# Kernel tuning notes

Hardware: AMD Instinct MI355X
Metric: run time of the kernel (lower is better)

The kernel has to match this reference:

```python
import jax, jax.numpy as jnp
import numpy as np

WH, WW = 7, 7
N = WH * WW
NH = 6
HEAD_DIM = 192 // NH
W_RES = 56
R_MAX = 4 * 56  # patch_size[0] * H
PI = 3.141592653589793


def _rel_coords():
    ch, cw = np.arange(WH), np.arange(WW)
    coords = np.stack(np.meshgrid(ch, cw, indexing='ij'))  # (2, WH, WW)
    flat = coords.reshape(2, -1)
    rel = flat[:, :, None] - flat[:, None, :]  # (2, N, N)
    radius = rel[0]   # in [-(WH-1), WH-1]
    azimuth = rel[1]  # in [-(WW-1), WW-1]
    return radius, azimuth


def setup_inputs() -> dict:
    key = jax.random.key(0)
    ks = jax.random.split(key, 10)
    B_ = 2048
    dim = 192
    return {
        'x': jax.random.normal(ks[0], (B_, N, dim), jnp.float32),
        'D': jax.random.uniform(ks[1], (B_, 1), jnp.float32),
        'qkv_w': jax.random.normal(ks[2], (3 * dim, dim), jnp.float32) * 0.02,
        'qkv_b': jax.random.normal(ks[3], (3 * dim,), jnp.float32) * 0.02,
        'proj_w': jax.random.normal(ks[4], (dim, dim), jnp.float32) * 0.02,
        'proj_b': jax.random.normal(ks[5], (dim,), jnp.float32) * 0.02,
        'a_p': jax.random.normal(ks[6], (2 * WW - 1, NH), jnp.float32) * 0.02,
        'b_p': jax.random.normal(ks[7], (2 * WW - 1, NH), jnp.float32) * 0.02,
        'a_r': jax.random.normal(ks[8], (2 * WH - 1, NH), jnp.float32) * 0.02,
        'b_r': jax.random.normal(ks[9], (2 * WH - 1, NH), jnp.float32) * 0.02,
    }


def reference(x, D, qkv_w, qkv_b, proj_w, proj_b, a_p, b_p, a_r, b_r):
    B_, n, C = x.shape
    radius_np, azimuth_np = _rel_coords()
    # torch a_r[radius] with negative ints wraps like python indexing; emulate via modulo
    rad_idx = jnp.asarray(radius_np % (2 * WH - 1))
    az_idx = jnp.asarray(azimuth_np % (2 * WW - 1))
    radius = jnp.asarray(radius_np, jnp.float32)   # (N, N)
    azimuth = jnp.asarray(azimuth_np, jnp.float32)  # (N, N)

    scale = HEAD_DIM ** -0.5
    qkv = (x @ qkv_w.T + qkv_b).reshape(B_, n, 3, NH, HEAD_DIM)
    qkv = jnp.transpose(qkv, (2, 0, 3, 1, 4))  # (3, B_, NH, N, hd)
    q, k, v = qkv[0] * scale, qkv[1], qkv[2]

    attn = jnp.einsum('bhnd,bhmd->bhnm', q, k)  # (B_, NH, N, N)

    # azimuthal bias: (N, N, NH) -> (NH, N, N)
    az = azimuth * (2.0 * PI / W_RES)
    A_phi = a_p[az_idx] * jnp.cos(az)[..., None] + b_p[az_idx] * jnp.sin(az)[..., None]
    A_phi = jnp.transpose(A_phi, (2, 0, 1))  # (NH, N, N)

    # radial bias: D (B_,1) scales radius -> (B_, N, N); combine -> (B_, NH, N, N)
    rad = D[:, 0][:, None, None] * radius[None]  # (B_, N, N)
    ang = rad * (2.0 * PI / R_MAX)
    A_r = (a_r[rad_idx][None] * jnp.cos(ang)[..., None]
           + b_r[rad_idx][None] * jnp.sin(ang)[..., None])  # (B_, N, N, NH)
    A_r = jnp.transpose(A_r, (0, 3, 1, 2))  # (B_, NH, N, N)

    attn = jax.nn.softmax(attn + A_phi[None] + A_r, axis=-1)
    out = jnp.einsum('bhnm,bhmd->bhnd', attn, v)
    out = jnp.transpose(out, (0, 2, 1, 3)).reshape(B_, n, C)
    return out @ proj_w.T + proj_b
```

## Files before the change

kernel.cpp:

```cpp
#include <hip/hip_runtime.h>

#define NTOK 49
#define NH 6
#define HD 32
#define DIM 192
#define QKV_DIM 576
#define PI_F 3.14159265358979323846f

typedef __bf16 bf16_t;
typedef __bf16 bf16x4 __attribute__((ext_vector_type(4)));
typedef __bf16 bf16x8 __attribute__((ext_vector_type(8)));
typedef float f32x4 __attribute__((ext_vector_type(4)));

__global__ __launch_bounds__(256) void cvt_weights(const float* __restrict__ qkv_w,
                                                   const float* __restrict__ proj_w,
                                                   bf16_t* __restrict__ wq,
                                                   bf16_t* __restrict__ wp) {
    int idx = blockIdx.x * 256 + threadIdx.x;
    if (idx < QKV_DIM * DIM) {
        wq[idx] = (bf16_t)qkv_w[idx];
    } else {
        int j = idx - QKV_DIM * DIM;
        if (j < DIM * DIM) wp[j] = (bf16_t)proj_w[j];
    }
}

__global__ __launch_bounds__(384) void fused_win_attn(
        const float* __restrict__ x,
        const float* __restrict__ Dp,
        const bf16_t* __restrict__ wq,
        const float* __restrict__ qkv_b,
        const bf16_t* __restrict__ wp,
        const float* __restrict__ proj_b,
        const float* __restrict__ a_p,
        const float* __restrict__ b_p,
        const float* __restrict__ a_r,
        const float* __restrict__ b_r,
        float* __restrict__ out) {
    __shared__ __align__(16) bf16_t sh_xo[64 * 200];
    __shared__ __align__(16) bf16_t q_sh[NH][64 * 40];
    __shared__ __align__(16) bf16_t k_sh[NH][64 * 40];
    __shared__ __align__(16) bf16_t vt_sh[NH][32 * 72];
    __shared__ __align__(16) bf16_t P_sh[NH][16 * 72];
    __shared__ float bias_sh[NH][169];

    const int tid  = threadIdx.x;
    const int w    = tid >> 6;
    const int lane = tid & 63;
    const int l16  = lane & 15;
    const int quad = lane >> 4;
    const int win  = blockIdx.x;

    bf16_t* q_lds  = q_sh[w];
    bf16_t* k_lds  = k_sh[w];
    bf16_t* vt     = vt_sh[w];
    bf16_t* P      = P_sh[w];
    float*  bias13 = bias_sh[w];

    const float* xg = x + (size_t)win * (NTOK * DIM);
    for (int u = tid; u < 2352; u += 384) {
        int e = u * 4;
        int r = e / 192, c = e % 192;
        float4 xv = *(const float4*)(xg + e);
        bf16x4 pk = { (bf16_t)xv.x, (bf16_t)xv.y, (bf16_t)xv.z, (bf16_t)xv.w };
        *(bf16x4*)(&sh_xo[r * 200 + c]) = pk;
    }
    {
        bf16x8 z = {};
        for (int u = tid; u < 360; u += 384) {
            int e = u * 8;
            int r = 49 + e / 192, c = e % 192;
            *(bf16x8*)(&sh_xo[r * 200 + c]) = z;
        }
    }
    __syncthreads();

    bf16x8 af[4][6];
#pragma unroll
    for (int mt = 0; mt < 4; ++mt)
#pragma unroll
        for (int ks = 0; ks < 6; ++ks)
            af[mt][ks] = *(const bf16x8*)(&sh_xo[(mt * 16 + l16) * 200 + ks * 32 + quad * 8]);
    __syncthreads();

    const float Dv = Dp[win];
    for (int u = lane; u < 169; u += 64) {
        int dr = u / 13 - 6, da = u % 13 - 6;
        int ri = (dr < 0) ? dr + 13 : dr;
        int ai = (da < 0) ? da + 13 : da;
        float ang_a = (float)da * (2.0f * PI_F / 56.0f);
        float ang_r = Dv * (float)dr * (2.0f * PI_F / 448.0f);
        bias13[u] = a_p[ai * NH + w] * __cosf(ang_a) + b_p[ai * NH + w] * __sinf(ang_a)
                  + a_r[ri * NH + w] * __cosf(ang_r) + b_r[ri * NH + w] * __sinf(ang_r);
    }

    const float scale = 0.17677669529663687f;
    for (int part = 0; part < 3; ++part) {
        const int base_c = part * DIM + w * 32;
        const bf16_t* wg = wq + (size_t)base_c * DIM;
        f32x4 acc[4][2] = {};
#pragma unroll
        for (int ks = 0; ks < 6; ++ks) {
            bf16x8 b0 = *(const bf16x8*)(wg + (size_t)l16 * DIM + ks * 32 + quad * 8);
            bf16x8 b1 = *(const bf16x8*)(wg + (size_t)(16 + l16) * DIM + ks * 32 + quad * 8);
#pragma unroll
            for (int mt = 0; mt < 4; ++mt) {
                acc[mt][0] = __builtin_amdgcn_mfma_f32_16x16x32_bf16(af[mt][ks], b0, acc[mt][0], 0, 0, 0);
                acc[mt][1] = __builtin_amdgcn_mfma_f32_16x16x32_bf16(af[mt][ks], b1, acc[mt][1], 0, 0, 0);
            }
        }
        float bb0 = qkv_b[base_c + l16];
        float bb1 = qkv_b[base_c + 16 + l16];
        if (part == 0) {
#pragma unroll
            for (int mt = 0; mt < 4; ++mt)
#pragma unroll
                for (int r = 0; r < 4; ++r) {
                    int tok = mt * 16 + quad * 4 + r;
                    q_lds[tok * 40 + l16]      = (bf16_t)((acc[mt][0][r] + bb0) * scale);
                    q_lds[tok * 40 + 16 + l16] = (bf16_t)((acc[mt][1][r] + bb1) * scale);
                }
        } else if (part == 1) {
#pragma unroll
            for (int mt = 0; mt < 4; ++mt)
#pragma unroll
                for (int r = 0; r < 4; ++r) {
                    int tok = mt * 16 + quad * 4 + r;
                    k_lds[tok * 40 + l16]      = (bf16_t)(acc[mt][0][r] + bb0);
                    k_lds[tok * 40 + 16 + l16] = (bf16_t)(acc[mt][1][r] + bb1);
                }
        } else {
#pragma unroll
            for (int mt = 0; mt < 4; ++mt)
#pragma unroll
                for (int r = 0; r < 4; ++r) {
                    int tok = mt * 16 + quad * 4 + r;
                    vt[(l16) * 72 + tok]      = (bf16_t)(acc[mt][0][r] + bb0);
                    vt[(16 + l16) * 72 + tok] = (bf16_t)(acc[mt][1][r] + bb1);
                }
        }
    }

    bf16x8 kf[4];
#pragma unroll
    for (int nt = 0; nt < 4; ++nt)
        kf[nt] = *(const bf16x8*)(&k_lds[(nt * 16 + l16) * 40 + quad * 8]);
    bf16x8 vf[2][2];
#pragma unroll
    for (int ntd = 0; ntd < 2; ++ntd)
#pragma unroll
        for (int kt = 0; kt < 2; ++kt)
            vf[ntd][kt] = *(const bf16x8*)(&vt[(ntd * 16 + l16) * 72 + kt * 32 + quad * 8]);

    int jh[4], jw[4];
#pragma unroll
    for (int nt = 0; nt < 4; ++nt) {
        int j = nt * 16 + l16;
        jh[nt] = j / 7;
        jw[nt] = j - 7 * jh[nt];
    }

    for (int mt = 0; mt < 4; ++mt) {
        bf16x8 qf = *(const bf16x8*)(&q_lds[(mt * 16 + l16) * 40 + quad * 8]);

        f32x4 s[4] = {};
#pragma unroll
        for (int nt = 0; nt < 4; ++nt)
            s[nt] = __builtin_amdgcn_mfma_f32_16x16x32_bf16(qf, kf[nt], s[nt], 0, 0, 0);

        float ev[4][4];
        float rs[4];
#pragma unroll
        for (int r = 0; r < 4; ++r) {
            int i = mt * 16 + quad * 4 + r;
            int ih = i / 7, iw = i - 7 * ih;
            float val[4];
            float mx = -1e30f;
#pragma unroll
            for (int nt = 0; nt < 4; ++nt) {
                int j = nt * 16 + l16;
                int idx = (ih - jh[nt] + 6) * 13 + (iw - jw[nt] + 6);
                idx = min(max(idx, 0), 168);
                float vv = s[nt][r] + bias13[idx];
                if (j >= 49) vv = -1e30f;
                val[nt] = vv;
                mx = fmaxf(mx, vv);
            }
#pragma unroll
            for (int m = 1; m <= 8; m <<= 1) mx = fmaxf(mx, __shfl_xor(mx, m));
            float sum = 0.f;
#pragma unroll
            for (int nt = 0; nt < 4; ++nt) {
                float e = __expf(val[nt] - mx);
                ev[r][nt] = e;
                sum += e;
            }
#pragma unroll
            for (int m = 1; m <= 8; m <<= 1) sum += __shfl_xor(sum, m);
            rs[r] = 1.0f / sum;
        }

#pragma unroll
        for (int r = 0; r < 4; ++r)
#pragma unroll
            for (int nt = 0; nt < 4; ++nt)
                P[(quad * 4 + r) * 72 + nt * 16 + l16] = (bf16_t)ev[r][nt];

        bf16x8 pa[2];
#pragma unroll
        for (int kt = 0; kt < 2; ++kt)
            pa[kt] = *(const bf16x8*)(&P[l16 * 72 + kt * 32 + quad * 8]);

        f32x4 o[2] = {};
#pragma unroll
        for (int ntd = 0; ntd < 2; ++ntd)
#pragma unroll
            for (int kt = 0; kt < 2; ++kt)
                o[ntd] = __builtin_amdgcn_mfma_f32_16x16x32_bf16(pa[kt], vf[ntd][kt], o[ntd], 0, 0, 0);

#pragma unroll
        for (int r = 0; r < 4; ++r) {
            int tok = mt * 16 + quad * 4 + r;
            bf16_t* op = &sh_xo[tok * 200 + w * 32];
            op[l16]      = (bf16_t)(o[0][r] * rs[r]);
            op[16 + l16] = (bf16_t)(o[1][r] * rs[r]);
        }
    }

    __syncthreads();

    bf16x8 wf[2][6];
#pragma unroll
    for (int nt = 0; nt < 2; ++nt)
#pragma unroll
        for (int ks = 0; ks < 6; ++ks)
            wf[nt][ks] = *(const bf16x8*)(wp + (size_t)(w * 32 + nt * 16 + l16) * DIM + ks * 32 + quad * 8);

    f32x4 pacc[4][2] = {};
#pragma unroll
    for (int mt = 0; mt < 4; ++mt)
#pragma unroll
        for (int ks = 0; ks < 6; ++ks) {
            bf16x8 oa = *(const bf16x8*)(&sh_xo[(mt * 16 + l16) * 200 + ks * 32 + quad * 8]);
#pragma unroll
            for (int nt = 0; nt < 2; ++nt)
                pacc[mt][nt] = __builtin_amdgcn_mfma_f32_16x16x32_bf16(oa, wf[nt][ks], pacc[mt][nt], 0, 0, 0);
        }

    float pb0 = proj_b[w * 32 + l16];
    float pb1 = proj_b[w * 32 + 16 + l16];
#pragma unroll
    for (int mt = 0; mt < 4; ++mt)
#pragma unroll
        for (int r = 0; r < 4; ++r) {
            int i = mt * 16 + quad * 4 + r;
            if (i < 49) {
                float* op = out + ((size_t)win * NTOK + i) * DIM + w * 32;
                op[l16]      = pacc[mt][0][r] + pb0;
                op[16 + l16] = pacc[mt][1][r] + pb1;
            }
        }
}

extern "C" void kernel_launch(void* const* d_in, const int* in_sizes, int n_in,
                              void* d_out, int out_size, void* d_ws, size_t ws_size,
                              hipStream_t stream) {
    const float* x      = (const float*)d_in[0];
    const float* D      = (const float*)d_in[1];
    const float* qkv_w  = (const float*)d_in[2];
    const float* qkv_b  = (const float*)d_in[3];
    const float* proj_w = (const float*)d_in[4];
    const float* proj_b = (const float*)d_in[5];
    const float* a_p    = (const float*)d_in[6];
    const float* b_p    = (const float*)d_in[7];
    const float* a_r    = (const float*)d_in[8];
    const float* b_r    = (const float*)d_in[9];
    float* out = (float*)d_out;

    const int B_ = in_sizes[0] / (NTOK * DIM);

    char* wsp = (char*)d_ws;
    bf16_t* wq = (bf16_t*)wsp; wsp += (size_t)QKV_DIM * DIM * 2;
    bf16_t* wp = (bf16_t*)wsp;

    cvt_weights<<<dim3((QKV_DIM * DIM + DIM * DIM + 255) / 256), dim3(256), 0, stream>>>(
        qkv_w, proj_w, wq, wp);

    fused_win_attn<<<dim3(B_), dim3(384), 0, stream>>>(
        x, D, wq, qkv_b, wp, proj_b, a_p, b_p, a_r, b_r, out);
}
```

Before: 293.2 us.

## Keep Q/K/P in registers via transposed MFMA and lane shuffles, shrink LDS

Computes Q and K transposed (weights as the A operand) and rebuilds their MFMA fragments with cross-lane shuffles instead of staging them through LDS. Softmax now runs down columns, and P is rebuilt through shuffles too, so the Q, K and P shared buffers go away. The x tile is no longer held in registers and is instead re-read from LDS with clamped rows. Launch bounds now request 3 blocks per CU. Together these cut LDS footprint and register pressure to raise occupancy, at the cost of more shuffle instructions and repeated LDS reads of x.

```diff
diff --git a/kernel.cpp b/kernel.cpp
--- a/kernel.cpp
+++ b/kernel.cpp
@@ -25,7 +25,27 @@
     }
 }
 
-__global__ __launch_bounds__(384) void fused_win_attn(
+__device__ __forceinline__ int2 pack4(float a, float b, float c, float d) {
+    bf16x4 t = { (bf16_t)a, (bf16_t)b, (bf16_t)c, (bf16_t)d };
+    union { bf16x4 v; int2 i; } u;
+    u.v = t;
+    return u.i;
+}
+
+__device__ __forceinline__ bf16x8 asm_frag(int2 p0, int2 p1, int src_lo, bool sel_hi) {
+    int a0x = __shfl(p0.x, src_lo),      a0y = __shfl(p0.y, src_lo);
+    int a1x = __shfl(p0.x, src_lo + 16), a1y = __shfl(p0.y, src_lo + 16);
+    int b0x = __shfl(p1.x, src_lo),      b0y = __shfl(p1.y, src_lo);
+    int b1x = __shfl(p1.x, src_lo + 16), b1y = __shfl(p1.y, src_lo + 16);
+    union { int x[4]; bf16x8 v; } u;
+    u.x[0] = sel_hi ? b0x : a0x;
+    u.x[1] = sel_hi ? b0y : a0y;
+    u.x[2] = sel_hi ? b1x : a1x;
+    u.x[3] = sel_hi ? b1y : a1y;
+    return u.v;
+}
+
+__global__ __launch_bounds__(384, 3) void fused_win_attn(
         const float* __restrict__ x,
         const float* __restrict__ Dp,
         const bf16_t* __restrict__ wq,
@@ -37,11 +57,8 @@
         const float* __restrict__ a_r,
         const float* __restrict__ b_r,
         float* __restrict__ out) {
-    __shared__ __align__(16) bf16_t sh_xo[64 * 200];
-    __shared__ __align__(16) bf16_t q_sh[NH][64 * 40];
-    __shared__ __align__(16) bf16_t k_sh[NH][64 * 40];
+    __shared__ __align__(16) bf16_t sh_xo[49 * 200];
     __shared__ __align__(16) bf16_t vt_sh[NH][32 * 72];
-    __shared__ __align__(16) bf16_t P_sh[NH][16 * 72];
     __shared__ float bias_sh[NH][169];
 
     const int tid  = threadIdx.x;
@@ -51,10 +68,7 @@
     const int quad = lane >> 4;
     const int win  = blockIdx.x;
 
-    bf16_t* q_lds  = q_sh[w];
-    bf16_t* k_lds  = k_sh[w];
     bf16_t* vt     = vt_sh[w];
-    bf16_t* P      = P_sh[w];
     float*  bias13 = bias_sh[w];
 
     const float* xg = x + (size_t)win * (NTOK * DIM);
@@ -65,23 +79,6 @@
         bf16x4 pk = { (bf16_t)xv.x, (bf16_t)xv.y, (bf16_t)xv.z, (bf16_t)xv.w };
         *(bf16x4*)(&sh_xo[r * 200 + c]) = pk;
     }
-    {
-        bf16x8 z = {};
-        for (int u = tid; u < 360; u += 384) {
-            int e = u * 8;
-            int r = 49 + e / 192, c = e % 192;
-            *(bf16x8*)(&sh_xo[r * 200 + c]) = z;
-        }
-    }
-    __syncthreads();
-
-    bf16x8 af[4][6];
-#pragma unroll
-    for (int mt = 0; mt < 4; ++mt)
-#pragma unroll
-        for (int ks = 0; ks < 6; ++ks)
-            af[mt][ks] = *(const bf16x8*)(&sh_xo[(mt * 16 + l16) * 200 + ks * 32 + quad * 8]);
-    __syncthreads();
 
     const float Dv = Dp[win];
     for (int u = lane; u < 169; u += 64) {
@@ -93,58 +90,85 @@
         bias13[u] = a_p[ai * NH + w] * __cosf(ang_a) + b_p[ai * NH + w] * __sinf(ang_a)
                   + a_r[ri * NH + w] * __cosf(ang_r) + b_r[ri * NH + w] * __sinf(ang_r);
     }
+    __syncthreads();
+
+    int xoff[4];
+#pragma unroll
+    for (int mt = 0; mt < 4; ++mt) {
+        int row = mt * 16 + l16;
+        xoff[mt] = min(row, 48) * 200 + quad * 8;
+    }
 
     const float scale = 0.17677669529663687f;
-    for (int part = 0; part < 3; ++part) {
-        const int base_c = part * DIM + w * 32;
-        const bf16_t* wg = wq + (size_t)base_c * DIM;
-        f32x4 acc[4][2] = {};
+    int2 qp[4][2], kp[4][2];
+    {
+        const bf16_t* wgq = wq + (size_t)(w * 32) * DIM;
+        const bf16_t* wgk = wq + (size_t)(DIM + w * 32) * DIM;
+        f32x4 qa[4][2] = {}, ka[4][2] = {};
 #pragma unroll
         for (int ks = 0; ks < 6; ++ks) {
-            bf16x8 b0 = *(const bf16x8*)(wg + (size_t)l16 * DIM + ks * 32 + quad * 8);
-            bf16x8 b1 = *(const bf16x8*)(wg + (size_t)(16 + l16) * DIM + ks * 32 + quad * 8);
+            bf16x8 wq0 = *(const bf16x8*)(wgq + (size_t)l16 * DIM + ks * 32 + quad * 8);
+            bf16x8 wq1 = *(const bf16x8*)(wgq + (size_t)(16 + l16) * DIM + ks * 32 + quad * 8);
+            bf16x8 wk0 = *(const bf16x8*)(wgk + (size_t)l16 * DIM + ks * 32 + quad * 8);
+            bf16x8 wk1 = *(const bf16x8*)(wgk + (size_t)(16 + l16) * DIM + ks * 32 + quad * 8);
 #pragma unroll
             for (int mt = 0; mt < 4; ++mt) {
-                acc[mt][0] = __builtin_amdgcn_mfma_f32_16x16x32_bf16(af[mt][ks], b0, acc[mt][0], 0, 0, 0);
-                acc[mt][1] = __builtin_amdgcn_mfma_f32_16x16x32_bf16(af[mt][ks], b1, acc[mt][1], 0, 0, 0);
-            }
-        }
-        float bb0 = qkv_b[base_c + l16];
-        float bb1 = qkv_b[base_c + 16 + l16];
-        if (part == 0) {
-#pragma unroll
-            for (int mt = 0; mt < 4; ++mt)
-#pragma unroll
-                for (int r = 0; r < 4; ++r) {
-                    int tok = mt * 16 + quad * 4 + r;
-                    q_lds[tok * 40 + l16]      = (bf16_t)((acc[mt][0][r] + bb0) * scale);
-                    q_lds[tok * 40 + 16 + l16] = (bf16_t)((acc[mt][1][r] + bb1) * scale);
-                }
-        } else if (part == 1) {
-#pragma unroll
-            for (int mt = 0; mt < 4; ++mt)
-#pragma unroll
-                for (int r = 0; r < 4; ++r) {
-                    int tok = mt * 16 + quad * 4 + r;
-                    k_lds[tok * 40 + l16]      = (bf16_t)(acc[mt][0][r] + bb0);
-                    k_lds[tok * 40 + 16 + l16] = (bf16_t)(acc[mt][1][r] + bb1);
-                }
-        } else {
-#pragma unroll
-            for (int mt = 0; mt < 4; ++mt)
-#pragma unroll
-                for (int r = 0; r < 4; ++r) {
-                    int tok = mt * 16 + quad * 4 + r;
-                    vt[(l16) * 72 + tok]      = (bf16_t)(acc[mt][0][r] + bb0);
-                    vt[(16 + l16) * 72 + tok] = (bf16_t)(acc[mt][1][r] + bb1);
-                }
-        }
-    }
-
-    bf16x8 kf[4];
-#pragma unroll
-    for (int nt = 0; nt < 4; ++nt)
-        kf[nt] = *(const bf16x8*)(&k_lds[(nt * 16 + l16) * 40 + quad * 8]);
+                bf16x8 xf = *(const bf16x8*)(&sh_xo[xoff[mt] + ks * 32]);
+                qa[mt][0] = __builtin_amdgcn_mfma_f32_16x16x32_bf16(wq0, xf, qa[mt][0], 0, 0, 0);
+                qa[mt][1] = __builtin_amdgcn_mfma_f32_16x16x32_bf16(wq1, xf, qa[mt][1], 0, 0, 0);
+                ka[mt][0] = __builtin_amdgcn_mfma_f32_16x16x32_bf16(wk0, xf, ka[mt][0], 0, 0, 0);
+                ka[mt][1] = __builtin_amdgcn_mfma_f32_16x16x32_bf16(wk1, xf, ka[mt][1], 0, 0, 0);
+            }
+        }
+        float4 bq0 = *(const float4*)(qkv_b + w * 32 + quad * 4);
+        float4 bq1 = *(const float4*)(qkv_b + w * 32 + 16 + quad * 4);
+        float4 bk0 = *(const float4*)(qkv_b + DIM + w * 32 + quad * 4);
+        float4 bk1 = *(const float4*)(qkv_b + DIM + w * 32 + 16 + quad * 4);
+#pragma unroll
+        for (int mt = 0; mt < 4; ++mt) {
+            qp[mt][0] = pack4((qa[mt][0][0] + bq0.x) * scale, (qa[mt][0][1] + bq0.y) * scale,
+                              (qa[mt][0][2] + bq0.z) * scale, (qa[mt][0][3] + bq0.w) * scale);
+            qp[mt][1] = pack4((qa[mt][1][0] + bq1.x) * scale, (qa[mt][1][1] + bq1.y) * scale,
+                              (qa[mt][1][2] + bq1.z) * scale, (qa[mt][1][3] + bq1.w) * scale);
+            kp[mt][0] = pack4(ka[mt][0][0] + bk0.x, ka[mt][0][1] + bk0.y,
+                              ka[mt][0][2] + bk0.z, ka[mt][0][3] + bk0.w);
+            kp[mt][1] = pack4(ka[mt][1][0] + bk1.x, ka[mt][1][1] + bk1.y,
+                              ka[mt][1][2] + bk1.z, ka[mt][1][3] + bk1.w);
+        }
+    }
+    {
+        const bf16_t* wgv = wq + (size_t)(2 * DIM + w * 32) * DIM;
+        f32x4 va[4][2] = {};
+#pragma unroll
+        for (int ks = 0; ks < 6; ++ks) {
+            bf16x8 wv0 = *(const bf16x8*)(wgv + (size_t)l16 * DIM + ks * 32 + quad * 8);
+            bf16x8 wv1 = *(const bf16x8*)(wgv + (size_t)(16 + l16) * DIM + ks * 32 + quad * 8);
+#pragma unroll
+            for (int mt = 0; mt < 4; ++mt) {
+                bf16x8 xf = *(const bf16x8*)(&sh_xo[xoff[mt] + ks * 32]);
+                va[mt][0] = __builtin_amdgcn_mfma_f32_16x16x32_bf16(xf, wv0, va[mt][0], 0, 0, 0);
+                va[mt][1] = __builtin_amdgcn_mfma_f32_16x16x32_bf16(xf, wv1, va[mt][1], 0, 0, 0);
+            }
+        }
+        float bv0 = qkv_b[2 * DIM + w * 32 + l16];
+        float bv1 = qkv_b[2 * DIM + w * 32 + 16 + l16];
+#pragma unroll
+        for (int mt = 0; mt < 4; ++mt) {
+            *(int2*)(&vt[l16 * 72 + mt * 16 + quad * 4]) =
+                pack4(va[mt][0][0] + bv0, va[mt][0][1] + bv0, va[mt][0][2] + bv0, va[mt][0][3] + bv0);
+            *(int2*)(&vt[(16 + l16) * 72 + mt * 16 + quad * 4]) =
+                pack4(va[mt][1][0] + bv1, va[mt][1][1] + bv1, va[mt][1][2] + bv1, va[mt][1][3] + bv1);
+        }
+    }
+
+    const int src_lo  = ((lane >> 4) & 1) * 32 + l16;
+    const bool sel_hi = (lane & 32) != 0;
+    bf16x8 qf[4], kf[4];
+#pragma unroll
+    for (int t = 0; t < 4; ++t) {
+        qf[t] = asm_frag(qp[t][0], qp[t][1], src_lo, sel_hi);
+        kf[t] = asm_frag(kp[t][0], kp[t][1], src_lo, sel_hi);
+    }
     bf16x8 vf[2][2];
 #pragma unroll
     for (int ntd = 0; ntd < 2; ++ntd)
@@ -152,78 +176,77 @@
         for (int kt = 0; kt < 2; ++kt)
             vf[ntd][kt] = *(const bf16x8*)(&vt[(ntd * 16 + l16) * 72 + kt * 32 + quad * 8]);
 
-    int jh[4], jw[4];
+    int jcp[4];
 #pragma unroll
     for (int nt = 0; nt < 4; ++nt) {
-        int j = nt * 16 + l16;
-        jh[nt] = j / 7;
-        jw[nt] = j - 7 * jh[nt];
-    }
+        int p = 0;
+#pragma unroll
+        for (int r = 0; r < 4; ++r) {
+            int j = nt * 16 + quad * 4 + r;
+            p |= ((j / 7) * 13 + (j % 7)) << (8 * r);
+        }
+        jcp[nt] = p;
+    }
+
+    __syncthreads();
 
     for (int mt = 0; mt < 4; ++mt) {
-        bf16x8 qf = *(const bf16x8*)(&q_lds[(mt * 16 + l16) * 40 + quad * 8]);
-
         f32x4 s[4] = {};
 #pragma unroll
         for (int nt = 0; nt < 4; ++nt)
-            s[nt] = __builtin_amdgcn_mfma_f32_16x16x32_bf16(qf, kf[nt], s[nt], 0, 0, 0);
-
-        float ev[4][4];
-        float rs[4];
-#pragma unroll
-        for (int r = 0; r < 4; ++r) {
-            int i = mt * 16 + quad * 4 + r;
-            int ih = i / 7, iw = i - 7 * ih;
-            float val[4];
-            float mx = -1e30f;
-#pragma unroll
-            for (int nt = 0; nt < 4; ++nt) {
-                int j = nt * 16 + l16;
-                int idx = (ih - jh[nt] + 6) * 13 + (iw - jw[nt] + 6);
-                idx = min(max(idx, 0), 168);
+            s[nt] = __builtin_amdgcn_mfma_f32_16x16x32_bf16(kf[nt], qf[mt], s[nt], 0, 0, 0);
+
+        int i = mt * 16 + l16;
+        int icl = min(i, 48);
+        int icode = (icl / 7) * 13 + (icl % 7) + 84;
+
+        float val[4][4];
+        float mx = -1e30f;
+#pragma unroll
+        for (int nt = 0; nt < 4; ++nt)
+#pragma unroll
+            for (int r = 0; r < 4; ++r) {
+                int j = nt * 16 + quad * 4 + r;
+                int idx = icode - ((jcp[nt] >> (8 * r)) & 255);
+                idx = max(idx, 0);
                 float vv = s[nt][r] + bias13[idx];
-                if (j >= 49) vv = -1e30f;
-                val[nt] = vv;
+                vv = (j < 49) ? vv : -1e30f;
+                val[nt][r] = vv;
                 mx = fmaxf(mx, vv);
             }
-#pragma unroll
-            for (int m = 1; m <= 8; m <<= 1) mx = fmaxf(mx, __shfl_xor(mx, m));
-            float sum = 0.f;
-#pragma unroll
-            for (int nt = 0; nt < 4; ++nt) {
-                float e = __expf(val[nt] - mx);
-                ev[r][nt] = e;
+        mx = fmaxf(mx, __shfl_xor(mx, 16));
+        mx = fmaxf(mx, __shfl_xor(mx, 32));
+        float sum = 0.f;
+#pragma unroll
+        for (int nt = 0; nt < 4; ++nt)
+#pragma unroll
+            for (int r = 0; r < 4; ++r) {
+                float e = __expf(val[nt][r] - mx);
+                val[nt][r] = e;
                 sum += e;
             }
-#pragma unroll
-            for (int m = 1; m <= 8; m <<= 1) sum += __shfl_xor(sum, m);
-            rs[r] = 1.0f / sum;
-        }
-
-#pragma unroll
-        for (int r = 0; r < 4; ++r)
-#pragma unroll
-            for (int nt = 0; nt < 4; ++nt)
-                P[(quad * 4 + r) * 72 + nt * 16 + l16] = (bf16_t)ev[r][nt];
-
-        bf16x8 pa[2];
-#pragma unroll
-        for (int kt = 0; kt < 2; ++kt)
-            pa[kt] = *(const bf16x8*)(&P[l16 * 72 + kt * 32 + quad * 8]);
-
-        f32x4 o[2] = {};
-#pragma unroll
-        for (int ntd = 0; ntd < 2; ++ntd)
-#pragma unroll
-            for (int kt = 0; kt < 2; ++kt)
-                o[ntd] = __builtin_amdgcn_mfma_f32_16x16x32_bf16(pa[kt], vf[ntd][kt], o[ntd], 0, 0, 0);
-
-#pragma unroll
-        for (int r = 0; r < 4; ++r) {
-            int tok = mt * 16 + quad * 4 + r;
-            bf16_t* op = &sh_xo[tok * 200 + w * 32];
-            op[l16]      = (bf16_t)(o[0][r] * rs[r]);
-            op[16 + l16] = (bf16_t)(o[1][r] * rs[r]);
+        sum += __shfl_xor(sum, 16);
+        sum += __shfl_xor(sum, 32);
+        float rs = 1.0f / sum;
+
+        int2 pv0 = pack4(val[0][0], val[0][1], val[0][2], val[0][3]);
+        int2 pv1 = pack4(val[1][0], val[1][1], val[1][2], val[1][3]);
+        int2 pv2 = pack4(val[2][0], val[2][1], val[2][2], val[2][3]);
+        int2 pv3 = pack4(val[3][0], val[3][1], val[3][2], val[3][3]);
+        bf16x8 pT0 = asm_frag(pv0, pv1, src_lo, sel_hi);
+        bf16x8 pT1 = asm_frag(pv2, pv3, src_lo, sel_hi);
+
+        f32x4 o0 = {}, o1 = {};
+        o0 = __builtin_amdgcn_mfma_f32_16x16x32_bf16(vf[0][0], pT0, o0, 0, 0, 0);
+        o0 = __builtin_amdgcn_mfma_f32_16x16x32_bf16(vf[0][1], pT1, o0, 0, 0, 0);
+        o1 = __builtin_amdgcn_mfma_f32_16x16x32_bf16(vf[1][0], pT0, o1, 0, 0, 0);
+        o1 = __builtin_amdgcn_mfma_f32_16x16x32_bf16(vf[1][1], pT1, o1, 0, 0, 0);
+
+        if (i < 49) {
+            *(int2*)(&sh_xo[i * 200 + w * 32 + quad * 4]) =
+                pack4(o0[0] * rs, o0[1] * rs, o0[2] * rs, o0[3] * rs);
+            *(int2*)(&sh_xo[i * 200 + w * 32 + 16 + quad * 4]) =
+                pack4(o1[0] * rs, o1[1] * rs, o1[2] * rs, o1[3] * rs);
         }
     }
 
@@ -241,10 +264,9 @@
     for (int mt = 0; mt < 4; ++mt)
 #pragma unroll
         for (int ks = 0; ks < 6; ++ks) {
-            bf16x8 oa = *(const bf16x8*)(&sh_xo[(mt * 16 + l16) * 200 + ks * 32 + quad * 8]);
-#pragma unroll
-            for (int nt = 0; nt < 2; ++nt)
-                pacc[mt][nt] = __builtin_amdgcn_mfma_f32_16x16x32_bf16(oa, wf[nt][ks], pacc[mt][nt], 0, 0, 0);
+            bf16x8 oa = *(const bf16x8*)(&sh_xo[xoff[mt] + ks * 32]);
+            pacc[mt][0] = __builtin_amdgcn_mfma_f32_16x16x32_bf16(oa, wf[0][ks], pacc[mt][0], 0, 0, 0);
+            pacc[mt][1] = __builtin_amdgcn_mfma_f32_16x16x32_bf16(oa, wf[1][ks], pacc[mt][1], 0, 0, 0);
         }
 
     float pb0 = proj_b[w * 32 + l16];
```

New measurement: 302.6 us. 1.03x slower.
